# Performance work log

Measured on AMD Instinct MI355X. Metric: run time of the kernel, lower is better.

Reference implementation:

```python
import jax, jax.numpy as jnp
import numpy as np

NUM_CLASSES = 81
B, P = 32, 32768

def setup_inputs() -> dict:
    key = jax.random.key(0)
    k1, k2, k3, k4, k5 = jax.random.split(key, 5)
    loc_t = jax.random.normal(k1, (B, P, 4), jnp.float32)
    loc_data = jax.random.normal(k2, (B, P, 4), jnp.float32)
    conf_data = jax.random.normal(k3, (B, P, NUM_CLASSES), jnp.float32)
    r = jax.random.uniform(k4, (B, P))
    cls = jax.random.randint(k5, (B, P), 1, NUM_CLASSES)
    conf_t = jnp.where(r < 0.02, cls, jnp.where(r < 0.04, -1, 0)).astype(jnp.int32)
    return {"loc_t": loc_t, "loc_data": loc_data, "conf_t": conf_t, "conf_data": conf_data}

def reference(loc_t, loc_data, conf_t, conf_data):
    num, num_priors, C = conf_data.shape
    pos = conf_t > 0           # [B,P] positive anchors
    regard = conf_t == -1      # [B,P] ignored anchors
    conf_t = jnp.where(regard, 0, conf_t)

    # ---- localization: smooth L1 over positive anchors, summed ----
    diff = jnp.abs(loc_data - loc_t)
    sl1 = jnp.where(diff < 1.0, 0.5 * diff * diff, diff - 0.5)
    loss_l = jnp.sum(sl1 * pos[..., None].astype(sl1.dtype))

    # ---- hard-negative mining score (log_sum_exp with GLOBAL max, as in source) ----
    m = jax.lax.stop_gradient(jnp.max(conf_data))
    lse_global = jnp.log(jnp.sum(jnp.exp(conf_data - m), axis=-1)) + m  # [B,P]
    gathered = jnp.take_along_axis(conf_data, conf_t[..., None], axis=-1)[..., 0]  # [B,P]
    loss_c = lse_global - gathered
    loss_c = jnp.where(pos | regard, 0.0, loss_c)

    # double argsort -> rank of each anchor in descending loss order
    order = jnp.argsort(-loss_c, axis=1)
    rank = jnp.argsort(order, axis=1)
    num_pos = jnp.sum(pos, axis=1, keepdims=True)                     # [B,1]
    num_neg = jnp.minimum(3 * num_pos, num_priors - 1)                # [B,1]
    neg = rank < num_neg                                              # [B,P]

    # ---- classification: cross-entropy over pos|neg anchors, summed ----
    ce = jax.nn.logsumexp(conf_data, axis=-1) - gathered              # [B,P]
    loss_conf = jnp.sum(jnp.where(pos | neg, ce, 0.0))

    N = jnp.sum(num_pos).astype(jnp.float32)
    return (loss_l / N, loss_conf / N)
```

## Files before the change

kernel.cpp:

```cpp
#include <hip/hip_runtime.h>
#include <cstdint>

#define NUM_CLASSES 81
#define BB 32
#define PP 32768
#define CA 64
#define TPB 256
#define CHUNK_FLOATS (CA * NUM_CLASSES)
#define CHUNK_F4 (CHUNK_FLOATS / 4)
#define NCHUNK (BB * PP / CA)
#define GRID_MAIN 768
#define NP_STRIDE 32

__device__ __forceinline__ unsigned f2key(float f) {
    unsigned u = __float_as_uint(f);
    return u ^ (unsigned)(((int)u >> 31) | (int)0x80000000u);
}
__device__ __forceinline__ float key2f(unsigned k) {
    unsigned u = (k & 0x80000000u) ? (k ^ 0x80000000u) : ~k;
    return __uint_as_float(u);
}


__global__ void mbl_zero_kernel(unsigned* __restrict__ p, int n) {
    int i = blockIdx.x * 256 + threadIdx.x;
    if (i < n) p[i] = 0u;
}

__global__ __launch_bounds__(TPB, 4) void mbl_main_kernel(
    const float* __restrict__ loc_t, const float* __restrict__ loc_data,
    const int* __restrict__ conf_t, const float* __restrict__ conf,
    float* __restrict__ loss_c, float* __restrict__ acc, int* __restrict__ num_pos)
{
    __shared__ __align__(16) float tile[2][CHUNK_FLOATS];
    __shared__ float wred[2][TPB / 64];

    const int t = threadIdx.x;
    const int lane = t & 63;
    const int w = t >> 6;
    const int q = lane >> 4;
    const int a_loc = (w << 4) | (lane & 15);

    float sum_ll = 0.f, sum_pce = 0.f;

    int c = blockIdx.x;
    {
        const float4* src = (const float4*)(conf + (size_t)c * CHUNK_FLOATS);
        float4* dst = (float4*)tile[0];
        #pragma unroll
        for (int i = 0; i < 5; ++i) dst[t + i * TPB] = src[t + i * TPB];
        if (t < CHUNK_F4 - 5 * TPB) dst[t + 5 * TPB] = src[t + 5 * TPB];
    }
    int parity = 0;
    const int stride = gridDim.x;
    for (; c < NCHUNK; c += stride) {
        __syncthreads();
        const int nc = c + stride;
        if (nc < NCHUNK) {
            const float4* src = (const float4*)(conf + (size_t)nc * CHUNK_FLOATS);
            float4* dst = (float4*)tile[parity ^ 1];
            #pragma unroll
            for (int i = 0; i < 5; ++i) dst[t + i * TPB] = src[t + i * TPB];
            if (t < CHUNK_F4 - 5 * TPB) dst[t + 5 * TPB] = src[t + 5 * TPB];
        }
        const float* cp = tile[parity] + a_loc * NUM_CLASSES + q * 20;
        float s = 0.f;
        #pragma unroll
        for (int j = 0; j < 20; ++j) s += __expf(cp[j]);
        if (q == 3) s += __expf(cp[20]);
        s += __shfl_xor(s, 16);
        s += __shfl_xor(s, 32);

        bool posl = false;
        if (q == 0) {
            const int idx = c * CA + a_loc;
            const int label = conf_t[idx];
            posl = label > 0;
            const bool regard = label == -1;
            const int lab = label < 0 ? 0 : label;
            const float g = tile[parity][a_loc * NUM_CLASSES + lab];
            const float ce = __logf(s) - g;
            loss_c[idx] = (posl || regard) ? 0.f : ce;
            if (posl) {
                float4 a4 = ((const float4*)loc_data)[idx];
                float4 b4 = ((const float4*)loc_t)[idx];
                float d0 = fabsf(a4.x - b4.x), d1 = fabsf(a4.y - b4.y);
                float d2 = fabsf(a4.z - b4.z), d3 = fabsf(a4.w - b4.w);
                sum_ll += (d0 < 1.f) ? 0.5f * d0 * d0 : d0 - 0.5f;
                sum_ll += (d1 < 1.f) ? 0.5f * d1 * d1 : d1 - 0.5f;
                sum_ll += (d2 < 1.f) ? 0.5f * d2 * d2 : d2 - 0.5f;
                sum_ll += (d3 < 1.f) ? 0.5f * d3 * d3 : d3 - 0.5f;
                sum_pce += ce;
            }
        }
        unsigned long long bal = __ballot(posl);
        if (lane == 0 && bal)
            atomicAdd(&num_pos[(c >> 9) * NP_STRIDE], (int)__popcll(bal));
        parity ^= 1;
    }
    #pragma unroll
    for (int off = 32; off > 0; off >>= 1) {
        sum_ll += __shfl_down(sum_ll, off);
        sum_pce += __shfl_down(sum_pce, off);
    }
    if (lane == 0) { wred[0][w] = sum_ll; wred[1][w] = sum_pce; }
    __syncthreads();
    if (t == 0) {
        float s0 = 0.f, s1 = 0.f;
        #pragma unroll
        for (int i = 0; i < TPB / 64; ++i) { s0 += wred[0][i]; s1 += wred[1][i]; }
        atomicAdd(&acc[0], s0);
        atomicAdd(&acc[1], s1);
    }
}

__global__ __launch_bounds__(256) void mbl_hist_kernel(
    const float* __restrict__ loss_c, const unsigned* __restrict__ prefix,
    unsigned* __restrict__ ghist, int shift, unsigned mask)
{
    const int b = blockIdx.x >> 4;
    const int slice = blockIdx.x & 15;
    const int t = threadIdx.x;
    __shared__ unsigned h[256];
    h[t] = 0u;
    __syncthreads();
    const unsigned pref = prefix[b];
    const float4* r4 = (const float4*)(loss_c + (size_t)b * PP + slice * 2048);
    #pragma unroll
    for (int i = 0; i < 2; ++i) {
        float4 v = r4[t + 256 * i];
        unsigned k0 = f2key(v.x), k1 = f2key(v.y), k2 = f2key(v.z), k3 = f2key(v.w);
        if ((k0 & mask) == pref) atomicAdd(&h[(k0 >> shift) & 255u], 1u);
        if ((k1 & mask) == pref) atomicAdd(&h[(k1 >> shift) & 255u], 1u);
        if ((k2 & mask) == pref) atomicAdd(&h[(k2 >> shift) & 255u], 1u);
        if ((k3 & mask) == pref) atomicAdd(&h[(k3 >> shift) & 255u], 1u);
    }
    __syncthreads();
    unsigned cnt = h[t];
    if (cnt) atomicAdd(&ghist[b * 256 + t], cnt);
}

__global__ __launch_bounds__(256) void mbl_pick_kernel(
    unsigned* __restrict__ ghist, unsigned* __restrict__ prefix,
    unsigned* __restrict__ remaining, const int* __restrict__ num_pos,
    int shift, int first)
{
    const int b = blockIdx.x;
    const int t = threadIdx.x;
    __shared__ unsigned suf[256];
    __shared__ unsigned sh_k;
    if (t == 0) {
        unsigned k;
        if (first) {
            int kk = 3 * num_pos[b * NP_STRIDE];
            if (kk > PP - 1) kk = PP - 1;
            if (kk <= 0) { prefix[b] = 0xFFFFFFFFu; remaining[b] = 0u; k = 0u; }
            else k = (unsigned)kk;
        } else {
            k = remaining[b];
        }
        sh_k = k;
    }
    __syncthreads();
    const unsigned krem = sh_k;
    if (krem == 0u) return;

    unsigned hv = ghist[b * 256 + t];
    ghist[b * 256 + t] = 0u;
    suf[t] = hv;
    __syncthreads();
    #pragma unroll
    for (int step = 1; step < 256; step <<= 1) {
        unsigned v = suf[t] + ((t + step < 256) ? suf[t + step] : 0u);
        __syncthreads();
        suf[t] = v;
        __syncthreads();
    }
    const unsigned above = (t == 255) ? 0u : suf[t + 1];
    if (suf[t] >= krem && above < krem) {
        prefix[b] |= ((unsigned)t) << shift;
        remaining[b] = krem - above;
    }
}

__global__ __launch_bounds__(256) void mbl_sum_kernel(
    const float* __restrict__ loss_c, const unsigned* __restrict__ prefix,
    float* __restrict__ acc)
{
    const int b = blockIdx.x >> 4;
    const int slice = blockIdx.x & 15;
    const int t = threadIdx.x;
    const int lane = t & 63;
    const int w = t >> 6;
    const unsigned T = prefix[b];
    const float4* r4 = (const float4*)(loss_c + (size_t)b * PP + slice * 2048);
    float partial = 0.f;
    #pragma unroll
    for (int i = 0; i < 2; ++i) {
        float4 v = r4[t + 256 * i];
        if (f2key(v.x) > T) partial += v.x;
        if (f2key(v.y) > T) partial += v.y;
        if (f2key(v.z) > T) partial += v.z;
        if (f2key(v.w) > T) partial += v.w;
    }
    #pragma unroll
    for (int off = 32; off > 0; off >>= 1) partial += __shfl_down(partial, off);
    __shared__ float r[4];
    if (lane == 0) r[w] = partial;
    __syncthreads();
    if (t == 0) atomicAdd(&acc[2], r[0] + r[1] + r[2] + r[3]);
}

__global__ void mbl_final_kernel(const float* __restrict__ acc,
                                 const int* __restrict__ num_pos,
                                 const unsigned* __restrict__ prefix,
                                 const unsigned* __restrict__ remaining,
                                 float* __restrict__ out)
{
    if (threadIdx.x == 0 && blockIdx.x == 0) {
        int n = 0;
        float extra = 0.f;
        for (int i = 0; i < BB; ++i) {
            n += num_pos[i * NP_STRIDE];
            unsigned rem = remaining[i];
            if (rem) extra += (float)rem * key2f(prefix[i]);
        }
        const float N = (float)n;
        out[0] = acc[0] / N;
        out[1] = (acc[1] + acc[2] + extra) / N;
    }
}

extern "C" void kernel_launch(void* const* d_in, const int* in_sizes, int n_in,
                              void* d_out, int out_size, void* d_ws, size_t ws_size,
                              hipStream_t stream) {
    const float* loc_t    = (const float*)d_in[0];
    const float* loc_data = (const float*)d_in[1];
    const int*   conf_t   = (const int*)d_in[2];
    const float* conf     = (const float*)d_in[3];
    float* out = (float*)d_out;

    char* ws = (char*)d_ws;
    const size_t off0 = (size_t)BB * PP * sizeof(float);
    float*    loss_c    = (float*)ws;
    float*    acc       = (float*)(ws + off0);
    int*      num_pos   = (int*)(ws + off0 + 256);
    unsigned* prefix    = (unsigned*)(ws + off0 + 4608);
    unsigned* remaining = (unsigned*)(ws + off0 + 4864);
    unsigned* ghist     = (unsigned*)(ws + off0 + 5120);

    mbl_zero_kernel<<<37, 256, 0, stream>>>((unsigned*)(ws + off0), 9472);

    mbl_main_kernel<<<GRID_MAIN, TPB, 0, stream>>>(
        loc_t, loc_data, conf_t, conf, loss_c, acc, num_pos);

    const unsigned masks[4] = {0x00000000u, 0xFF000000u, 0xFFFF0000u, 0xFFFFFF00u};
    for (int p = 0; p < 4; ++p) {
        const int shift = 24 - 8 * p;
        mbl_hist_kernel<<<512, 256, 0, stream>>>(loss_c, prefix, ghist, shift, masks[p]);
        mbl_pick_kernel<<<BB, 256, 0, stream>>>(ghist, prefix, remaining, num_pos,
                                                shift, p == 0 ? 1 : 0);
    }
    mbl_sum_kernel<<<512, 256, 0, stream>>>(loss_c, prefix, acc);
    mbl_final_kernel<<<1, 64, 0, stream>>>(acc, num_pos, prefix, remaining, out);
}
```

Before: 513.1 us.

## Fuse radix top-k select into one per-batch kernel and use direct global-to-LDS loads

Replaces the eight alternating histogram and pick launches plus the sum kernel with a single 1024-thread block per batch row. Each block holds its 32768 keys in registers, builds per-wave LDS histograms across four radix passes, and sums the selected values, removing repeated global reads of loss_c and several launch gaps. The main kernel's conf tile staging now uses global_load_lds instead of loads through registers, and the zero kernel shrinks to one block. The risks are that only 32 blocks run the selection, which may leave most CUs idle, and that 32 key registers per thread add register pressure.

```diff
diff --git a/kernel.cpp b/kernel.cpp
--- a/kernel.cpp
+++ b/kernel.cpp
@@ -12,6 +12,11 @@
 #define GRID_MAIN 768
 #define NP_STRIDE 32
 
+#define GLDS16(g, s)                                              \
+    __builtin_amdgcn_global_load_lds(                             \
+        (const __attribute__((address_space(1))) void*)(g),       \
+        (__attribute__((address_space(3))) void*)(s), 16, 0, 0)
+
 __device__ __forceinline__ unsigned f2key(float f) {
     unsigned u = __float_as_uint(f);
     return u ^ (unsigned)(((int)u >> 31) | (int)0x80000000u);
@@ -23,8 +28,7 @@
 
 
 __global__ void mbl_zero_kernel(unsigned* __restrict__ p, int n) {
-    int i = blockIdx.x * 256 + threadIdx.x;
-    if (i < n) p[i] = 0u;
+    for (int i = threadIdx.x; i < n; i += 256) p[i] = 0u;
 }
 
 __global__ __launch_bounds__(TPB, 4) void mbl_main_kernel(
@@ -45,11 +49,16 @@
 
     int c = blockIdx.x;
     {
-        const float4* src = (const float4*)(conf + (size_t)c * CHUNK_FLOATS);
-        float4* dst = (float4*)tile[0];
-        #pragma unroll
-        for (int i = 0; i < 5; ++i) dst[t + i * TPB] = src[t + i * TPB];
-        if (t < CHUNK_F4 - 5 * TPB) dst[t + 5 * TPB] = src[t + 5 * TPB];
+        const float* src = conf + (size_t)c * CHUNK_FLOATS;
+        #pragma unroll
+        for (int i = 0; i < 5; ++i) {
+            const int f = t + i * TPB;
+            GLDS16(src + f * 4, &tile[0][f * 4]);
+        }
+        if (t < CHUNK_F4 - 5 * TPB) {
+            const int f = t + 5 * TPB;
+            GLDS16(src + f * 4, &tile[0][f * 4]);
+        }
     }
     int parity = 0;
     const int stride = gridDim.x;
@@ -57,11 +66,17 @@
         __syncthreads();
         const int nc = c + stride;
         if (nc < NCHUNK) {
-            const float4* src = (const float4*)(conf + (size_t)nc * CHUNK_FLOATS);
-            float4* dst = (float4*)tile[parity ^ 1];
+            const float* src = conf + (size_t)nc * CHUNK_FLOATS;
+            float* dst = tile[parity ^ 1];
             #pragma unroll
-            for (int i = 0; i < 5; ++i) dst[t + i * TPB] = src[t + i * TPB];
-            if (t < CHUNK_F4 - 5 * TPB) dst[t + 5 * TPB] = src[t + 5 * TPB];
+            for (int i = 0; i < 5; ++i) {
+                const int f = t + i * TPB;
+                GLDS16(src + f * 4, dst + f * 4);
+            }
+            if (t < CHUNK_F4 - 5 * TPB) {
+                const int f = t + 5 * TPB;
+                GLDS16(src + f * 4, dst + f * 4);
+            }
         }
         const float* cp = tile[parity] + a_loc * NUM_CLASSES + q * 20;
         float s = 0.f;
@@ -114,120 +129,103 @@
     }
 }
 
-__global__ __launch_bounds__(256) void mbl_hist_kernel(
-    const float* __restrict__ loss_c, const unsigned* __restrict__ prefix,
-    unsigned* __restrict__ ghist, int shift, unsigned mask)
-{
-    const int b = blockIdx.x >> 4;
-    const int slice = blockIdx.x & 15;
-    const int t = threadIdx.x;
-    __shared__ unsigned h[256];
-    h[t] = 0u;
-    __syncthreads();
-    const unsigned pref = prefix[b];
-    const float4* r4 = (const float4*)(loss_c + (size_t)b * PP + slice * 2048);
-    #pragma unroll
-    for (int i = 0; i < 2; ++i) {
-        float4 v = r4[t + 256 * i];
-        unsigned k0 = f2key(v.x), k1 = f2key(v.y), k2 = f2key(v.z), k3 = f2key(v.w);
-        if ((k0 & mask) == pref) atomicAdd(&h[(k0 >> shift) & 255u], 1u);
-        if ((k1 & mask) == pref) atomicAdd(&h[(k1 >> shift) & 255u], 1u);
-        if ((k2 & mask) == pref) atomicAdd(&h[(k2 >> shift) & 255u], 1u);
-        if ((k3 & mask) == pref) atomicAdd(&h[(k3 >> shift) & 255u], 1u);
-    }
-    __syncthreads();
-    unsigned cnt = h[t];
-    if (cnt) atomicAdd(&ghist[b * 256 + t], cnt);
-}
-
-__global__ __launch_bounds__(256) void mbl_pick_kernel(
-    unsigned* __restrict__ ghist, unsigned* __restrict__ prefix,
-    unsigned* __restrict__ remaining, const int* __restrict__ num_pos,
-    int shift, int first)
+__global__ __launch_bounds__(1024, 1) void mbl_select_kernel(
+    const float* __restrict__ loss_c, const int* __restrict__ num_pos,
+    float* __restrict__ acc)
 {
     const int b = blockIdx.x;
     const int t = threadIdx.x;
+    const int w = t >> 6;
+
+    __shared__ unsigned hw_[16][256];
     __shared__ unsigned suf[256];
-    __shared__ unsigned sh_k;
+    __shared__ unsigned sh_digit, sh_rem, sh_k;
+    __shared__ float wsum[16];
+
     if (t == 0) {
-        unsigned k;
-        if (first) {
-            int kk = 3 * num_pos[b * NP_STRIDE];
-            if (kk > PP - 1) kk = PP - 1;
-            if (kk <= 0) { prefix[b] = 0xFFFFFFFFu; remaining[b] = 0u; k = 0u; }
-            else k = (unsigned)kk;
-        } else {
-            k = remaining[b];
-        }
-        sh_k = k;
+        int kk = 3 * num_pos[b * NP_STRIDE];
+        if (kk > PP - 1) kk = PP - 1;
+        sh_k = (kk <= 0) ? 0u : (unsigned)kk;
+    }
+
+    unsigned key[32];
+    const float4* r4 = (const float4*)(loss_c + (size_t)b * PP);
+    #pragma unroll
+    for (int i = 0; i < 8; ++i) {
+        float4 v = r4[t + i * 1024];
+        key[4 * i + 0] = f2key(v.x); key[4 * i + 1] = f2key(v.y);
+        key[4 * i + 2] = f2key(v.z); key[4 * i + 3] = f2key(v.w);
     }
     __syncthreads();
-    const unsigned krem = sh_k;
+    unsigned krem = sh_k;
     if (krem == 0u) return;
 
-    unsigned hv = ghist[b * 256 + t];
-    ghist[b * 256 + t] = 0u;
-    suf[t] = hv;
+    unsigned pref = 0u;
+    #pragma unroll
+    for (int p = 0; p < 4; ++p) {
+        const int shift = 24 - 8 * p;
+        const unsigned mask = (p == 0) ? 0u : (0xFFFFFFFFu << (shift + 8));
+
+        #pragma unroll
+        for (int i = 0; i < 4; ++i) ((unsigned*)hw_)[t + i * 1024] = 0u;
+        __syncthreads();
+        #pragma unroll
+        for (int j = 0; j < 32; ++j)
+            if ((key[j] & mask) == pref)
+                atomicAdd(&hw_[w][(key[j] >> shift) & 255u], 1u);
+        __syncthreads();
+        if (t < 256) {
+            unsigned s = 0u;
+            #pragma unroll
+            for (int i = 0; i < 16; ++i) s += hw_[i][t];
+            suf[t] = s;
+        }
+        __syncthreads();
+        for (int step = 1; step < 256; step <<= 1) {
+            unsigned v = 0u;
+            if (t < 256) v = suf[t] + ((t + step < 256) ? suf[t + step] : 0u);
+            __syncthreads();
+            if (t < 256) suf[t] = v;
+            __syncthreads();
+        }
+        if (t < 256) {
+            unsigned above = (t == 255) ? 0u : suf[t + 1];
+            if (suf[t] >= krem && above < krem) {
+                sh_digit = (unsigned)t;
+                sh_rem = krem - above;
+            }
+        }
+        __syncthreads();
+        pref |= sh_digit << shift;
+        krem = sh_rem;
+    }
+    float partial = 0.f;
+    #pragma unroll
+    for (int j = 0; j < 32; ++j)
+        if (key[j] > pref) partial += key2f(key[j]);
+    #pragma unroll
+    for (int off = 32; off > 0; off >>= 1) partial += __shfl_down(partial, off);
+    if ((t & 63) == 0) wsum[w] = partial;
     __syncthreads();
-    #pragma unroll
-    for (int step = 1; step < 256; step <<= 1) {
-        unsigned v = suf[t] + ((t + step < 256) ? suf[t + step] : 0u);
-        __syncthreads();
-        suf[t] = v;
-        __syncthreads();
-    }
-    const unsigned above = (t == 255) ? 0u : suf[t + 1];
-    if (suf[t] >= krem && above < krem) {
-        prefix[b] |= ((unsigned)t) << shift;
-        remaining[b] = krem - above;
-    }
-}
-
-__global__ __launch_bounds__(256) void mbl_sum_kernel(
-    const float* __restrict__ loss_c, const unsigned* __restrict__ prefix,
-    float* __restrict__ acc)
-{
-    const int b = blockIdx.x >> 4;
-    const int slice = blockIdx.x & 15;
-    const int t = threadIdx.x;
-    const int lane = t & 63;
-    const int w = t >> 6;
-    const unsigned T = prefix[b];
-    const float4* r4 = (const float4*)(loss_c + (size_t)b * PP + slice * 2048);
-    float partial = 0.f;
-    #pragma unroll
-    for (int i = 0; i < 2; ++i) {
-        float4 v = r4[t + 256 * i];
-        if (f2key(v.x) > T) partial += v.x;
-        if (f2key(v.y) > T) partial += v.y;
-        if (f2key(v.z) > T) partial += v.z;
-        if (f2key(v.w) > T) partial += v.w;
-    }
-    #pragma unroll
-    for (int off = 32; off > 0; off >>= 1) partial += __shfl_down(partial, off);
-    __shared__ float r[4];
-    if (lane == 0) r[w] = partial;
-    __syncthreads();
-    if (t == 0) atomicAdd(&acc[2], r[0] + r[1] + r[2] + r[3]);
+    if (t == 0) {
+        float s = 0.f;
+        #pragma unroll
+        for (int i = 0; i < 16; ++i) s += wsum[i];
+        s += (float)krem * key2f(pref);
+        atomicAdd(&acc[2], s);
+    }
 }
 
 __global__ void mbl_final_kernel(const float* __restrict__ acc,
                                  const int* __restrict__ num_pos,
-                                 const unsigned* __restrict__ prefix,
-                                 const unsigned* __restrict__ remaining,
                                  float* __restrict__ out)
 {
     if (threadIdx.x == 0 && blockIdx.x == 0) {
         int n = 0;
-        float extra = 0.f;
-        for (int i = 0; i < BB; ++i) {
-            n += num_pos[i * NP_STRIDE];
-            unsigned rem = remaining[i];
-            if (rem) extra += (float)rem * key2f(prefix[i]);
-        }
+        for (int i = 0; i < BB; ++i) n += num_pos[i * NP_STRIDE];
         const float N = (float)n;
         out[0] = acc[0] / N;
-        out[1] = (acc[1] + acc[2] + extra) / N;
+        out[1] = (acc[1] + acc[2]) / N;
     }
 }
 
@@ -242,25 +240,16 @@
 
     char* ws = (char*)d_ws;
     const size_t off0 = (size_t)BB * PP * sizeof(float);
-    float*    loss_c    = (float*)ws;
-    float*    acc       = (float*)(ws + off0);
-    int*      num_pos   = (int*)(ws + off0 + 256);
-    unsigned* prefix    = (unsigned*)(ws + off0 + 4608);
-    unsigned* remaining = (unsigned*)(ws + off0 + 4864);
-    unsigned* ghist     = (unsigned*)(ws + off0 + 5120);
-
-    mbl_zero_kernel<<<37, 256, 0, stream>>>((unsigned*)(ws + off0), 9472);
+    float* loss_c  = (float*)ws;
+    float* acc     = (float*)(ws + off0);
+    int*   num_pos = (int*)(ws + off0 + 256);
+
+    mbl_zero_kernel<<<1, 256, 0, stream>>>((unsigned*)(ws + off0), 1088);
 
     mbl_main_kernel<<<GRID_MAIN, TPB, 0, stream>>>(
         loc_t, loc_data, conf_t, conf, loss_c, acc, num_pos);
 
-    const unsigned masks[4] = {0x00000000u, 0xFF000000u, 0xFFFF0000u, 0xFFFFFF00u};
-    for (int p = 0; p < 4; ++p) {
-        const int shift = 24 - 8 * p;
-        mbl_hist_kernel<<<512, 256, 0, stream>>>(loss_c, prefix, ghist, shift, masks[p]);
-        mbl_pick_kernel<<<BB, 256, 0, stream>>>(ghist, prefix, remaining, num_pos,
-                                                shift, p == 0 ? 1 : 0);
-    }
-    mbl_sum_kernel<<<512, 256, 0, stream>>>(loss_c, prefix, acc);
-    mbl_final_kernel<<<1, 64, 0, stream>>>(acc, num_pos, prefix, remaining, out);
-}
+    mbl_select_kernel<<<BB, 1024, 0, stream>>>(loss_c, num_pos, acc);
+
+    mbl_final_kernel<<<1, 64, 0, stream>>>(acc, num_pos, out);
+}
```

After: 521.9 us. No clear change (+1.7%).
